# Kernel optimization log

Measured on AMD Instinct MI355X. Metric: run time of the kernel, lower is better.

The kernel has to match this reference:

```python
import jax, jax.numpy as jnp
import numpy as np

DIM = 1024
E = 8
K = 2
EPS = 1e-5

def _ln(x, g, b):
    mu = jnp.mean(x, axis=-1, keepdims=True)
    var = jnp.mean(jnp.square(x - mu), axis=-1, keepdims=True)
    return (x - mu) * jax.lax.rsqrt(var + EPS) * g + b

def setup_inputs() -> dict:
    key = jax.random.key(0)
    ks = jax.random.split(key, 8)
    H = 2 * DIM
    s_in = 1.0 / np.sqrt(DIM)
    s_h = 1.0 / np.sqrt(H)
    return {
        "x": jax.random.normal(ks[0], (2, 2048, DIM), dtype=jnp.float32),
        "gate_w": jax.random.uniform(ks[1], (DIM, E), minval=-s_in, maxval=s_in, dtype=jnp.float32),
        "w1": jax.random.uniform(ks[2], (E, DIM, H), minval=-s_in, maxval=s_in, dtype=jnp.float32),
        "b1": jax.random.uniform(ks[3], (E, H), minval=-s_in, maxval=s_in, dtype=jnp.float32),
        "ln1_g": jnp.ones((E, H), dtype=jnp.float32),
        "ln1_b": jnp.zeros((E, H), dtype=jnp.float32),
        "w2": jax.random.uniform(ks[4], (E, H, DIM), minval=-s_h, maxval=s_h, dtype=jnp.float32),
        "b2": jax.random.uniform(ks[5], (E, DIM), minval=-s_h, maxval=s_h, dtype=jnp.float32),
        "ln_g": jnp.ones((DIM,), dtype=jnp.float32),
        "ln_b": jnp.zeros((DIM,), dtype=jnp.float32),
    }

def reference(x, gate_w, w1, b1, ln1_g, ln1_b, w2, b2, ln_g, ln_b):
    shape = x.shape
    xf = x.reshape(-1, shape[-1])                      # [T, D]
    gates = jax.nn.softmax(xf @ gate_w, axis=-1)       # [T, E]
    topw, topi = jax.lax.top_k(gates, K)               # [T, K]
    topw = topw / jnp.sum(topw, axis=-1, keepdims=True)
    # combine weights per expert: [T, E]
    combine = jnp.sum(topw[:, :, None] * jax.nn.one_hot(topi, E, dtype=xf.dtype), axis=1)
    # run all experts on all tokens (vectorized grouped GEMM), combine by gate mask
    h = jnp.einsum('td,edh->teh', xf, w1) + b1          # [T, E, 2D]
    h = _ln(h, ln1_g, ln1_b)
    h = jax.nn.gelu(h, approximate=False)
    y = jnp.einsum('teh,ehd->ted', h, w2) + b2          # [T, E, D]
    out = jnp.einsum('ted,te->td', y, combine)          # [T, D]
    out = _ln(out + xf, ln_g, ln_b)
    return out.reshape(shape)
```

## Files before the change

kernel.cpp:

```cpp
#include <hip/hip_runtime.h>
#include <hip/hip_bf16.h>

#define DIMX 1024
#define HID  2048
#define NE   8
#define NT   4096
#define NPAIR 8192

typedef __attribute__((ext_vector_type(8))) __bf16 bf16x8;
typedef __attribute__((ext_vector_type(4))) float f32x4;

__device__ inline unsigned short f2bf(float f) {
  union { float f; unsigned u; } v; v.f = f;
  unsigned r = v.u + 0x7FFFu + ((v.u >> 16) & 1u);
  return (unsigned short)(r >> 16);
}
__device__ inline float bf2f(unsigned short h) {
  union { unsigned u; float f; } v; v.u = ((unsigned)h) << 16;
  return v.f;
}

__device__ __forceinline__ void gload_lds16(const unsigned short* g, unsigned short* l) {
  __builtin_amdgcn_global_load_lds(
      (const __attribute__((address_space(1))) unsigned int*)g,
      (__attribute__((address_space(3))) unsigned int*)l, 16, 0, 0);
}

#define O_CNT   0u
#define O_OFFS  256u
#define O_TOK   1024u
#define O_TK    (O_TOK + 131072u)
#define O_PW    (O_TK + 131072u)
#define O_TI    (O_PW + 131072u)
#define O_TW    (O_TI + 32768u)
#define O_XBF   524288u
#define O_W1T   16777216u
#define O_W2T   50331648u
#define O_H     83886080u
#define O_Y     117440512u

__global__ __launch_bounds__(64) void k_gate_top2(const float* __restrict__ x,
                                                  const float* __restrict__ gw,
                                                  int* __restrict__ ti,
                                                  float* __restrict__ tw) {
  int t = blockIdx.x;
  int lane = threadIdx.x;
  float p[NE];
#pragma unroll
  for (int e = 0; e < NE; e++) p[e] = 0.f;
  const float* xr = x + (size_t)t * DIMX;
  for (int j = 0; j < DIMX / 64; j++) {
    int d = lane + j * 64;
    float xv = xr[d];
    const float4* g4 = (const float4*)(gw + (size_t)d * NE);
    float4 a = g4[0], b = g4[1];
    p[0] += xv * a.x; p[1] += xv * a.y; p[2] += xv * a.z; p[3] += xv * a.w;
    p[4] += xv * b.x; p[5] += xv * b.y; p[6] += xv * b.z; p[7] += xv * b.w;
  }
#pragma unroll
  for (int e = 0; e < NE; e++)
#pragma unroll
    for (int off = 32; off > 0; off >>= 1) p[e] += __shfl_xor(p[e], off);
  if (lane == 0) {
    int ia = 0; float va = p[0];
#pragma unroll
    for (int e = 1; e < NE; e++) if (p[e] > va) { va = p[e]; ia = e; }
    int ib = -1; float vb = -3.0e38f;
#pragma unroll
    for (int e = 0; e < NE; e++) { if (e == ia) continue; if (p[e] > vb) { vb = p[e]; ib = e; } }
    float w0 = 1.f / (1.f + expf(vb - va));
    ti[t * 2] = ia;     tw[t * 2] = w0;
    ti[t * 2 + 1] = ib; tw[t * 2 + 1] = 1.f - w0;
  }
}

__global__ __launch_bounds__(512) void k_build(const int* __restrict__ ti,
                                               const float* __restrict__ tw,
                                               int* __restrict__ cnt, int* __restrict__ offs,
                                               int* __restrict__ ptok, int* __restrict__ ptk,
                                               float* __restrict__ pw) {
  __shared__ int scnt[NE];
  __shared__ int soffs[NE + 1];
  int wid = threadIdx.x >> 6;
  int lane = threadIdx.x & 63;
  int c = 0;
  for (int p = lane; p < NPAIR; p += 64) c += (ti[p] == wid) ? 1 : 0;
#pragma unroll
  for (int off = 32; off > 0; off >>= 1) c += __shfl_xor(c, off);
  if (lane == 0) scnt[wid] = c;
  __syncthreads();
  if (threadIdx.x == 0) {
    int s = 0;
    for (int e = 0; e < NE; e++) { soffs[e] = s; s += scnt[e]; }
    soffs[NE] = s;
  }
  __syncthreads();
  if (threadIdx.x < NE) {
    cnt[threadIdx.x] = scnt[threadIdx.x];
    offs[threadIdx.x] = soffs[threadIdx.x];
  }
  if (threadIdx.x == 0) offs[NE] = soffs[NE];
  int base = 0;
  for (int p0 = 0; p0 < NPAIR; p0 += 64) {
    int p = p0 + lane;
    bool m = (ti[p] == wid);
    unsigned long long mask = __ballot(m);
    if (m) {
      int pos = base + __popcll(mask & ((1ull << lane) - 1ull));
      ptok[wid * NT + pos] = p >> 1;
      ptk[wid * NT + pos] = p;
      pw[wid * NT + pos] = tw[p];
    }
    base += __popcll(mask);
  }
}

__global__ __launch_bounds__(256) void k_transpose_cvt(const float* __restrict__ in,
                                                       unsigned short* __restrict__ out,
                                                       int R, int C) {
  __shared__ float tile[32][33];
  int e = blockIdx.z;
  const float* ip = in + (size_t)e * R * C;
  unsigned short* op = out + (size_t)e * R * C;
  int tx = threadIdx.x & 31, ty = threadIdx.x >> 5;
  int c = blockIdx.x * 32 + tx;
  int r0 = blockIdx.y * 32;
#pragma unroll
  for (int i = 0; i < 4; i++) tile[ty + i * 8][tx] = ip[(size_t)(r0 + ty + i * 8) * C + c];
  __syncthreads();
  int r = r0 + tx;
#pragma unroll
  for (int i = 0; i < 4; i++)
    op[(size_t)(blockIdx.x * 32 + ty + i * 8) * R + r] = f2bf(tile[tx][ty + i * 8]);
}

__global__ __launch_bounds__(256) void k_cvt(const float* __restrict__ in,
                                             unsigned short* __restrict__ out, int n4) {
  int i = blockIdx.x * blockDim.x + threadIdx.x;
  if (i < n4) {
    float4 v = ((const float4*)in)[i];
    ushort4 o; o.x = f2bf(v.x); o.y = f2bf(v.y); o.z = f2bf(v.z); o.w = f2bf(v.w);
    ((ushort4*)out)[i] = o;
  }
}

#define BM 128
#define BN 128
#define BK 32

__global__ __launch_bounds__(256) void k_gemm1(
    const unsigned short* __restrict__ xbf,
    const unsigned short* __restrict__ w1t,
    const float* __restrict__ bias1,
    const int* __restrict__ cnt, const int* __restrict__ offs,
    const int* __restrict__ ptok,
    unsigned short* __restrict__ hpre)
{
  int e = blockIdx.z;
  int n_e = cnt[e];
  int row0 = blockIdx.y * BM;
  if (row0 >= n_e) return;
  int col0 = blockIdx.x * BN;
  int offs_e = offs[e];

  __shared__ __align__(16) unsigned short As[BM][BK];
  __shared__ __align__(16) unsigned short Bs[BN][BK];

  int tid = threadIdx.x;
  int lane = tid & 63, wid = tid >> 6;
  int wr = wid >> 1, wc = wid & 1;
  int quad = lane >> 4, m16 = lane & 15;

  int i4 = lane >> 2, kc = lane & 3;
  int ga0 = row0 + wid * 32 + i4;      if (ga0 >= n_e) ga0 = n_e - 1;
  int ga1 = row0 + wid * 32 + 16 + i4; if (ga1 >= n_e) ga1 = n_e - 1;
  int t0 = ptok[e * NT + ga0];
  int t1 = ptok[e * NT + ga1];
  const unsigned short* a0p = xbf + (size_t)t0 * DIMX + kc * 8;
  const unsigned short* a1p = xbf + (size_t)t1 * DIMX + kc * 8;
  const unsigned short* bb = w1t + (size_t)e * HID * DIMX;
  const unsigned short* b0p = bb + (size_t)(col0 + wid * 32 + i4) * DIMX + kc * 8;
  const unsigned short* b1p = bb + (size_t)(col0 + wid * 32 + 16 + i4) * DIMX + kc * 8;
  unsigned short* lA0 = &As[wid * 32][0];
  unsigned short* lA1 = &As[wid * 32 + 16][0];
  unsigned short* lB0 = &Bs[wid * 32][0];
  unsigned short* lB1 = &Bs[wid * 32 + 16][0];

  f32x4 acc[4][4];
#pragma unroll
  for (int i = 0; i < 4; i++)
#pragma unroll
    for (int j = 0; j < 4; j++) acc[i][j] = (f32x4)(0.f);

  for (int k0 = 0; k0 < DIMX; k0 += BK) {
    __syncthreads();
    gload_lds16(a0p + k0, lA0);
    gload_lds16(a1p + k0, lA1);
    gload_lds16(b0p + k0, lB0);
    gload_lds16(b1p + k0, lB1);
    __syncthreads();
    bf16x8 af[4], bfr[4];
#pragma unroll
    for (int i = 0; i < 4; i++) af[i]  = *(const bf16x8*)&As[wr * 64 + i * 16 + m16][quad * 8];
#pragma unroll
    for (int i = 0; i < 4; i++) bfr[i] = *(const bf16x8*)&Bs[wc * 64 + i * 16 + m16][quad * 8];
#pragma unroll
    for (int i = 0; i < 4; i++)
#pragma unroll
      for (int j = 0; j < 4; j++)
        acc[i][j] = __builtin_amdgcn_mfma_f32_16x16x32_bf16(af[i], bfr[j], acc[i][j], 0, 0, 0);
  }

#pragma unroll
  for (int i = 0; i < 4; i++) {
#pragma unroll
    for (int r = 0; r < 4; r++) {
      int rl = wr * 64 + i * 16 + quad * 4 + r;
      int g = row0 + rl;
      if (g < n_e) {
        size_t rowbase = (size_t)(offs_e + g) * HID;
#pragma unroll
        for (int j = 0; j < 4; j++) {
          int colg = col0 + wc * 64 + j * 16 + m16;
          float val = acc[i][j][r] + bias1[e * HID + colg];
          hpre[rowbase + colg] = f2bf(val);
        }
      }
    }
  }
}

__global__ __launch_bounds__(256) void k_ln_gelu(unsigned short* __restrict__ h,
                                                 const float* __restrict__ g1,
                                                 const float* __restrict__ bb1,
                                                 const int* __restrict__ offs) {
  __shared__ float sbuf[4];
  int row = blockIdx.x;
  int tid = threadIdx.x;
  int e = 0;
#pragma unroll
  for (int i = 1; i < NE; i++) if (row >= offs[i]) e = i;
  unsigned short* p = h + (size_t)row * HID;
  float v[8];
#pragma unroll
  for (int i = 0; i < 8; i++) v[i] = bf2f(p[tid + i * 256]);
  float s = 0.f;
#pragma unroll
  for (int i = 0; i < 8; i++) s += v[i];
#pragma unroll
  for (int off = 32; off > 0; off >>= 1) s += __shfl_xor(s, off);
  if ((tid & 63) == 0) sbuf[tid >> 6] = s;
  __syncthreads();
  float mean = (sbuf[0] + sbuf[1] + sbuf[2] + sbuf[3]) * (1.f / HID);
  float sq = 0.f;
#pragma unroll
  for (int i = 0; i < 8; i++) { float d = v[i] - mean; sq += d * d; }
#pragma unroll
  for (int off = 32; off > 0; off >>= 1) sq += __shfl_xor(sq, off);
  __syncthreads();
  if ((tid & 63) == 0) sbuf[tid >> 6] = sq;
  __syncthreads();
  float var = (sbuf[0] + sbuf[1] + sbuf[2] + sbuf[3]) * (1.f / HID);
  float rstd = rsqrtf(var + 1e-5f);
#pragma unroll
  for (int i = 0; i < 8; i++) {
    int d = tid + i * 256;
    float xn = (v[i] - mean) * rstd * g1[(size_t)e * HID + d] + bb1[(size_t)e * HID + d];
    float ge = 0.5f * xn * (1.f + erff(xn * 0.7071067811865476f));
    p[d] = f2bf(ge);
  }
}

__global__ __launch_bounds__(256) void k_gemm2(
    const unsigned short* __restrict__ hb,
    const unsigned short* __restrict__ w2t,
    const float* __restrict__ bias2,
    const int* __restrict__ cnt, const int* __restrict__ offs,
    const int* __restrict__ ptk, const float* __restrict__ pw,
    float* __restrict__ ybuf)
{
  int e = blockIdx.z;
  int n_e = cnt[e];
  int row0 = blockIdx.y * BM;
  if (row0 >= n_e) return;
  int col0 = blockIdx.x * BN;
  int offs_e = offs[e];

  __shared__ __align__(16) unsigned short As[BM][BK];
  __shared__ __align__(16) unsigned short Bs[BN][BK];

  int tid = threadIdx.x;
  int lane = tid & 63, wid = tid >> 6;
  int wr = wid >> 1, wc = wid & 1;
  int quad = lane >> 4, m16 = lane & 15;

  int i4 = lane >> 2, kc = lane & 3;
  int ga0 = row0 + wid * 32 + i4;      if (ga0 >= n_e) ga0 = n_e - 1;
  int ga1 = row0 + wid * 32 + 16 + i4; if (ga1 >= n_e) ga1 = n_e - 1;
  const unsigned short* a0p = hb + (size_t)(offs_e + ga0) * HID + kc * 8;
  const unsigned short* a1p = hb + (size_t)(offs_e + ga1) * HID + kc * 8;
  const unsigned short* bb = w2t + (size_t)e * DIMX * HID;
  const unsigned short* b0p = bb + (size_t)(col0 + wid * 32 + i4) * HID + kc * 8;
  const unsigned short* b1p = bb + (size_t)(col0 + wid * 32 + 16 + i4) * HID + kc * 8;
  unsigned short* lA0 = &As[wid * 32][0];
  unsigned short* lA1 = &As[wid * 32 + 16][0];
  unsigned short* lB0 = &Bs[wid * 32][0];
  unsigned short* lB1 = &Bs[wid * 32 + 16][0];

  f32x4 acc[4][4];
#pragma unroll
  for (int i = 0; i < 4; i++)
#pragma unroll
    for (int j = 0; j < 4; j++) acc[i][j] = (f32x4)(0.f);

  for (int k0 = 0; k0 < HID; k0 += BK) {
    __syncthreads();
    gload_lds16(a0p + k0, lA0);
    gload_lds16(a1p + k0, lA1);
    gload_lds16(b0p + k0, lB0);
    gload_lds16(b1p + k0, lB1);
    __syncthreads();
    bf16x8 af[4], bfr[4];
#pragma unroll
    for (int i = 0; i < 4; i++) af[i]  = *(const bf16x8*)&As[wr * 64 + i * 16 + m16][quad * 8];
#pragma unroll
    for (int i = 0; i < 4; i++) bfr[i] = *(const bf16x8*)&Bs[wc * 64 + i * 16 + m16][quad * 8];
#pragma unroll
    for (int i = 0; i < 4; i++)
#pragma unroll
      for (int j = 0; j < 4; j++)
        acc[i][j] = __builtin_amdgcn_mfma_f32_16x16x32_bf16(af[i], bfr[j], acc[i][j], 0, 0, 0);
  }

#pragma unroll
  for (int i = 0; i < 4; i++) {
#pragma unroll
    for (int r = 0; r < 4; r++) {
      int rl = wr * 64 + i * 16 + quad * 4 + r;
      int g = row0 + rl;
      if (g < n_e) {
        int pi = e * NT + g;
        float w = pw[pi];
        size_t obase = (size_t)ptk[pi] * DIMX;
#pragma unroll
        for (int j = 0; j < 4; j++) {
          int colg = col0 + wc * 64 + j * 16 + m16;
          ybuf[obase + colg] = (acc[i][j][r] + bias2[e * DIMX + colg]) * w;
        }
      }
    }
  }
}

__global__ __launch_bounds__(256) void k_final(const float* __restrict__ yb,
                                               const float* __restrict__ x,
                                               const float* __restrict__ lg,
                                               const float* __restrict__ lb,
                                               float* __restrict__ out) {
  __shared__ float sbuf[4];
  int t = blockIdx.x, tid = threadIdx.x;
  const float4* y0 = (const float4*)(yb + (size_t)t * 2 * DIMX);
  const float4* y1 = y0 + DIMX / 4;
  const float4* x4 = (const float4*)(x + (size_t)t * DIMX);
  float4 a = y0[tid], b = y1[tid], c = x4[tid];
  float4 v; v.x = a.x + b.x + c.x; v.y = a.y + b.y + c.y;
  v.z = a.z + b.z + c.z; v.w = a.w + b.w + c.w;
  float s = v.x + v.y + v.z + v.w;
#pragma unroll
  for (int off = 32; off > 0; off >>= 1) s += __shfl_xor(s, off);
  if ((tid & 63) == 0) sbuf[tid >> 6] = s;
  __syncthreads();
  float mean = (sbuf[0] + sbuf[1] + sbuf[2] + sbuf[3]) * (1.f / DIMX);
  float dx = v.x - mean, dy = v.y - mean, dz = v.z - mean, dw = v.w - mean;
  float sq = dx * dx + dy * dy + dz * dz + dw * dw;
#pragma unroll
  for (int off = 32; off > 0; off >>= 1) sq += __shfl_xor(sq, off);
  __syncthreads();
  if ((tid & 63) == 0) sbuf[tid >> 6] = sq;
  __syncthreads();
  float var = (sbuf[0] + sbuf[1] + sbuf[2] + sbuf[3]) * (1.f / DIMX);
  float rstd = rsqrtf(var + 1e-5f);
  float4 g = ((const float4*)lg)[tid], bb = ((const float4*)lb)[tid];
  float4 o; o.x = dx * rstd * g.x + bb.x; o.y = dy * rstd * g.y + bb.y;
  o.z = dz * rstd * g.z + bb.z; o.w = dw * rstd * g.w + bb.w;
  ((float4*)(out + (size_t)t * DIMX))[tid] = o;
}

extern "C" void kernel_launch(void* const* d_in, const int* in_sizes, int n_in,
                              void* d_out, int out_size, void* d_ws, size_t ws_size,
                              hipStream_t stream) {
  const float* x     = (const float*)d_in[0];
  const float* gw    = (const float*)d_in[1];
  const float* w1    = (const float*)d_in[2];
  const float* b1    = (const float*)d_in[3];
  const float* ln1g  = (const float*)d_in[4];
  const float* ln1b  = (const float*)d_in[5];
  const float* w2    = (const float*)d_in[6];
  const float* b2    = (const float*)d_in[7];
  const float* lng   = (const float*)d_in[8];
  const float* lnb   = (const float*)d_in[9];
  float* out = (float*)d_out;

  char* ws = (char*)d_ws;
  int* cnt  = (int*)(ws + O_CNT);
  int* offs = (int*)(ws + O_OFFS);
  int* ptok = (int*)(ws + O_TOK);
  int* ptk  = (int*)(ws + O_TK);
  float* pw = (float*)(ws + O_PW);
  int* ti   = (int*)(ws + O_TI);
  float* tw = (float*)(ws + O_TW);
  unsigned short* xbf = (unsigned short*)(ws + O_XBF);
  unsigned short* w1t = (unsigned short*)(ws + O_W1T);
  unsigned short* w2t = (unsigned short*)(ws + O_W2T);
  unsigned short* hpre = (unsigned short*)(ws + O_H);
  float* ybuf = (float*)(ws + O_Y);

  hipLaunchKernelGGL(k_gate_top2, dim3(NT), dim3(64), 0, stream, x, gw, ti, tw);
  hipLaunchKernelGGL(k_build, dim3(1), dim3(512), 0, stream, ti, tw, cnt, offs, ptok, ptk, pw);
  hipLaunchKernelGGL(k_cvt, dim3(NT * DIMX / 4 / 256), dim3(256), 0, stream, x, xbf, NT * DIMX / 4);
  hipLaunchKernelGGL(k_transpose_cvt, dim3(HID / 32, DIMX / 32, NE), dim3(256), 0, stream,
                     w1, w1t, DIMX, HID);
  hipLaunchKernelGGL(k_transpose_cvt, dim3(DIMX / 32, HID / 32, NE), dim3(256), 0, stream,
                     w2, w2t, HID, DIMX);
  hipLaunchKernelGGL(k_gemm1, dim3(HID / BN, NT / BM, NE), dim3(256), 0, stream,
                     xbf, w1t, b1, cnt, offs, ptok, hpre);
  hipLaunchKernelGGL(k_ln_gelu, dim3(NPAIR), dim3(256), 0, stream, hpre, ln1g, ln1b, offs);
  hipLaunchKernelGGL(k_gemm2, dim3(DIMX / BN, NT / BM, NE), dim3(256), 0, stream,
                     hpre, w2t, b2, cnt, offs, ptk, pw, ybuf);
  hipLaunchKernelGGL(k_final, dim3(NT), dim3(256), 0, stream, ybuf, x, lng, lnb, out);
}
```

Before: 415.8 us.

## Compact grouped-GEMM grid into per-expert strip list and fuse x conversion into gating

Replaces the dense (col, NT/BM, NE) GEMM grids, where most blocks exit early, with a compact list of 128-row strips built in k_build, padding each expert's rows to a multiple of 128. The bf16 conversion of x is fused into the gating kernel. The weight transpose uses 64x64 tiles with vectorized loads and stores, and LN+GELU is vectorized and looks up its expert from the strip table. This removes many empty blocks and one launch, in exchange for a serial strip-building step and padded row space that the LN kernel has to skip.

```diff
diff --git a/kernel.cpp b/kernel.cpp
--- a/kernel.cpp
+++ b/kernel.cpp
@@ -6,6 +6,7 @@
 #define NE   8
 #define NT   4096
 #define NPAIR 8192
+#define MAXSTRIP 72
 
 typedef __attribute__((ext_vector_type(8))) __bf16 bf16x8;
 typedef __attribute__((ext_vector_type(4))) float f32x4;
@@ -27,35 +28,49 @@
 }
 
 #define O_CNT   0u
-#define O_OFFS  256u
 #define O_TOK   1024u
-#define O_TK    (O_TOK + 131072u)
-#define O_PW    (O_TK + 131072u)
-#define O_TI    (O_PW + 131072u)
-#define O_TW    (O_TI + 32768u)
+#define O_TK    132096u
+#define O_PW    263168u
+#define O_TI    394240u
+#define O_TW    427008u
+#define O_POFF  459776u
+#define O_SE    459904u
+#define O_SR0   460416u
 #define O_XBF   524288u
 #define O_W1T   16777216u
 #define O_W2T   50331648u
 #define O_H     83886080u
-#define O_Y     117440512u
-
-__global__ __launch_bounds__(64) void k_gate_top2(const float* __restrict__ x,
+#define O_Y     121634816u
+
+__global__ __launch_bounds__(256) void k_gate_cvt(const float* __restrict__ x,
                                                   const float* __restrict__ gw,
+                                                  unsigned short* __restrict__ xbf,
                                                   int* __restrict__ ti,
                                                   float* __restrict__ tw) {
-  int t = blockIdx.x;
-  int lane = threadIdx.x;
+  int t = blockIdx.x * 4 + (threadIdx.x >> 6);
+  int lane = threadIdx.x & 63;
+  const float4* xr = (const float4*)(x + (size_t)t * DIMX);
+  ushort4* xo = (ushort4*)(xbf + (size_t)t * DIMX);
   float p[NE];
 #pragma unroll
   for (int e = 0; e < NE; e++) p[e] = 0.f;
-  const float* xr = x + (size_t)t * DIMX;
-  for (int j = 0; j < DIMX / 64; j++) {
-    int d = lane + j * 64;
-    float xv = xr[d];
-    const float4* g4 = (const float4*)(gw + (size_t)d * NE);
-    float4 a = g4[0], b = g4[1];
-    p[0] += xv * a.x; p[1] += xv * a.y; p[2] += xv * a.z; p[3] += xv * a.w;
-    p[4] += xv * b.x; p[5] += xv * b.y; p[6] += xv * b.z; p[7] += xv * b.w;
+#pragma unroll
+  for (int j = 0; j < 4; j++) {
+    int idx4 = j * 64 + lane;
+    float4 v = xr[idx4];
+    ushort4 o; o.x = f2bf(v.x); o.y = f2bf(v.y); o.z = f2bf(v.z); o.w = f2bf(v.w);
+    xo[idx4] = o;
+    const float4* gp = (const float4*)(gw + (size_t)(idx4 * 4) * NE);
+    float4 gA = gp[0], gB = gp[1], gC = gp[2], gD = gp[3];
+    float4 gE = gp[4], gF = gp[5], gG = gp[6], gH = gp[7];
+    p[0] += v.x * gA.x + v.y * gC.x + v.z * gE.x + v.w * gG.x;
+    p[1] += v.x * gA.y + v.y * gC.y + v.z * gE.y + v.w * gG.y;
+    p[2] += v.x * gA.z + v.y * gC.z + v.z * gE.z + v.w * gG.z;
+    p[3] += v.x * gA.w + v.y * gC.w + v.z * gE.w + v.w * gG.w;
+    p[4] += v.x * gB.x + v.y * gD.x + v.z * gF.x + v.w * gH.x;
+    p[5] += v.x * gB.y + v.y * gD.y + v.z * gF.y + v.w * gH.y;
+    p[6] += v.x * gB.z + v.y * gD.z + v.z * gF.z + v.w * gH.z;
+    p[7] += v.x * gB.w + v.y * gD.w + v.z * gF.w + v.w * gH.w;
   }
 #pragma unroll
   for (int e = 0; e < NE; e++)
@@ -76,34 +91,39 @@
 
 __global__ __launch_bounds__(512) void k_build(const int* __restrict__ ti,
                                                const float* __restrict__ tw,
-                                               int* __restrict__ cnt, int* __restrict__ offs,
+                                               int* __restrict__ cnt,
+                                               int* __restrict__ poffs,
+                                               int* __restrict__ s_e, int* __restrict__ s_r0,
                                                int* __restrict__ ptok, int* __restrict__ ptk,
                                                float* __restrict__ pw) {
+  __shared__ int sti[NPAIR];
   __shared__ int scnt[NE];
-  __shared__ int soffs[NE + 1];
+  for (int i = threadIdx.x; i < NPAIR; i += 512) sti[i] = ti[i];
+  __syncthreads();
   int wid = threadIdx.x >> 6;
   int lane = threadIdx.x & 63;
   int c = 0;
-  for (int p = lane; p < NPAIR; p += 64) c += (ti[p] == wid) ? 1 : 0;
+  for (int p = lane; p < NPAIR; p += 64) c += (sti[p] == wid) ? 1 : 0;
 #pragma unroll
   for (int off = 32; off > 0; off >>= 1) c += __shfl_xor(c, off);
   if (lane == 0) scnt[wid] = c;
   __syncthreads();
   if (threadIdx.x == 0) {
-    int s = 0;
-    for (int e = 0; e < NE; e++) { soffs[e] = s; s += scnt[e]; }
-    soffs[NE] = s;
-  }
-  __syncthreads();
-  if (threadIdx.x < NE) {
-    cnt[threadIdx.x] = scnt[threadIdx.x];
-    offs[threadIdx.x] = soffs[threadIdx.x];
-  }
-  if (threadIdx.x == 0) offs[NE] = soffs[NE];
+    int s = 0, pacc = 0;
+    for (int e = 0; e < NE; e++) {
+      cnt[e] = scnt[e];
+      poffs[e] = pacc;
+      int ns = (scnt[e] + 127) >> 7;
+      for (int k = 0; k < ns; k++) { s_e[s] = e; s_r0[s] = k * 128; s++; }
+      pacc += ns * 128;
+    }
+    poffs[NE] = pacc;
+    for (; s < MAXSTRIP; s++) { s_e[s] = -1; s_r0[s] = 0; }
+  }
   int base = 0;
   for (int p0 = 0; p0 < NPAIR; p0 += 64) {
     int p = p0 + lane;
-    bool m = (ti[p] == wid);
+    bool m = (sti[p] == wid);
     unsigned long long mask = __ballot(m);
     if (m) {
       int pos = base + __popcll(mask & ((1ull << lane) - 1ull));
@@ -118,29 +138,29 @@
 __global__ __launch_bounds__(256) void k_transpose_cvt(const float* __restrict__ in,
                                                        unsigned short* __restrict__ out,
                                                        int R, int C) {
-  __shared__ float tile[32][33];
+  __shared__ float tile[64][73];
   int e = blockIdx.z;
   const float* ip = in + (size_t)e * R * C;
   unsigned short* op = out + (size_t)e * R * C;
-  int tx = threadIdx.x & 31, ty = threadIdx.x >> 5;
-  int c = blockIdx.x * 32 + tx;
-  int r0 = blockIdx.y * 32;
-#pragma unroll
-  for (int i = 0; i < 4; i++) tile[ty + i * 8][tx] = ip[(size_t)(r0 + ty + i * 8) * C + c];
-  __syncthreads();
-  int r = r0 + tx;
-#pragma unroll
-  for (int i = 0; i < 4; i++)
-    op[(size_t)(blockIdx.x * 32 + ty + i * 8) * R + r] = f2bf(tile[tx][ty + i * 8]);
-}
-
-__global__ __launch_bounds__(256) void k_cvt(const float* __restrict__ in,
-                                             unsigned short* __restrict__ out, int n4) {
-  int i = blockIdx.x * blockDim.x + threadIdx.x;
-  if (i < n4) {
-    float4 v = ((const float4*)in)[i];
-    ushort4 o; o.x = f2bf(v.x); o.y = f2bf(v.y); o.z = f2bf(v.z); o.w = f2bf(v.w);
-    ((ushort4*)out)[i] = o;
+  int c0 = blockIdx.x * 64, r0 = blockIdx.y * 64;
+  int tx = threadIdx.x & 15, ty = threadIdx.x >> 4;
+#pragma unroll
+  for (int i = 0; i < 4; i++) {
+    int row = ty + i * 16;
+    float4 v = *(const float4*)(ip + (size_t)(r0 + row) * C + c0 + tx * 4);
+    tile[row][tx * 4] = v.x; tile[row][tx * 4 + 1] = v.y;
+    tile[row][tx * 4 + 2] = v.z; tile[row][tx * 4 + 3] = v.w;
+  }
+  __syncthreads();
+  int rx = threadIdx.x & 15, cy = threadIdx.x >> 4;
+  int r_off = rx * 4;
+#pragma unroll
+  for (int i = 0; i < 4; i++) {
+    int cc = cy + i * 16;
+    ushort4 h;
+    h.x = f2bf(tile[r_off][cc]);     h.y = f2bf(tile[r_off + 1][cc]);
+    h.z = f2bf(tile[r_off + 2][cc]); h.w = f2bf(tile[r_off + 3][cc]);
+    *(ushort4*)(op + (size_t)(c0 + cc) * R + r0 + r_off) = h;
   }
 }
 
@@ -152,16 +172,18 @@
     const unsigned short* __restrict__ xbf,
     const unsigned short* __restrict__ w1t,
     const float* __restrict__ bias1,
-    const int* __restrict__ cnt, const int* __restrict__ offs,
+    const int* __restrict__ cnt, const int* __restrict__ s_e,
+    const int* __restrict__ s_r0, const int* __restrict__ poffs,
     const int* __restrict__ ptok,
     unsigned short* __restrict__ hpre)
 {
-  int e = blockIdx.z;
+  int s = blockIdx.y;
+  int e = s_e[s];
+  if (e < 0) return;
+  int r0e = s_r0[s];
   int n_e = cnt[e];
-  int row0 = blockIdx.y * BM;
-  if (row0 >= n_e) return;
+  int pbase = poffs[e];
   int col0 = blockIdx.x * BN;
-  int offs_e = offs[e];
 
   __shared__ __align__(16) unsigned short As[BM][BK];
   __shared__ __align__(16) unsigned short Bs[BN][BK];
@@ -172,8 +194,8 @@
   int quad = lane >> 4, m16 = lane & 15;
 
   int i4 = lane >> 2, kc = lane & 3;
-  int ga0 = row0 + wid * 32 + i4;      if (ga0 >= n_e) ga0 = n_e - 1;
-  int ga1 = row0 + wid * 32 + 16 + i4; if (ga1 >= n_e) ga1 = n_e - 1;
+  int ga0 = r0e + wid * 32 + i4;      if (ga0 >= n_e) ga0 = n_e - 1;
+  int ga1 = r0e + wid * 32 + 16 + i4; if (ga1 >= n_e) ga1 = n_e - 1;
   int t0 = ptok[e * NT + ga0];
   int t1 = ptok[e * NT + ga1];
   const unsigned short* a0p = xbf + (size_t)t0 * DIMX + kc * 8;
@@ -215,10 +237,9 @@
   for (int i = 0; i < 4; i++) {
 #pragma unroll
     for (int r = 0; r < 4; r++) {
-      int rl = wr * 64 + i * 16 + quad * 4 + r;
-      int g = row0 + rl;
+      int g = r0e + wr * 64 + i * 16 + quad * 4 + r;
       if (g < n_e) {
-        size_t rowbase = (size_t)(offs_e + g) * HID;
+        size_t rowbase = (size_t)(pbase + g) * HID;
 #pragma unroll
         for (int j = 0; j < 4; j++) {
           int colg = col0 + wc * 64 + j * 16 + m16;
@@ -233,17 +254,18 @@
 __global__ __launch_bounds__(256) void k_ln_gelu(unsigned short* __restrict__ h,
                                                  const float* __restrict__ g1,
                                                  const float* __restrict__ bb1,
-                                                 const int* __restrict__ offs) {
+                                                 const int* __restrict__ s_e) {
   __shared__ float sbuf[4];
   int row = blockIdx.x;
+  int e = s_e[row >> 7];
+  if (e < 0) return;
   int tid = threadIdx.x;
-  int e = 0;
-#pragma unroll
-  for (int i = 1; i < NE; i++) if (row >= offs[i]) e = i;
   unsigned short* p = h + (size_t)row * HID;
+  ushort4 u0 = ((const ushort4*)p)[tid * 2];
+  ushort4 u1 = ((const ushort4*)p)[tid * 2 + 1];
   float v[8];
-#pragma unroll
-  for (int i = 0; i < 8; i++) v[i] = bf2f(p[tid + i * 256]);
+  v[0] = bf2f(u0.x); v[1] = bf2f(u0.y); v[2] = bf2f(u0.z); v[3] = bf2f(u0.w);
+  v[4] = bf2f(u1.x); v[5] = bf2f(u1.y); v[6] = bf2f(u1.z); v[7] = bf2f(u1.w);
   float s = 0.f;
 #pragma unroll
   for (int i = 0; i < 8; i++) s += v[i];
@@ -262,29 +284,41 @@
   __syncthreads();
   float var = (sbuf[0] + sbuf[1] + sbuf[2] + sbuf[3]) * (1.f / HID);
   float rstd = rsqrtf(var + 1e-5f);
+  const float4* gg = (const float4*)(g1 + (size_t)e * HID);
+  const float4* gb = (const float4*)(bb1 + (size_t)e * HID);
+  float4 ga = gg[tid * 2], gbv = gg[tid * 2 + 1];
+  float4 ba = gb[tid * 2], bbv = gb[tid * 2 + 1];
+  float gn[8] = {ga.x, ga.y, ga.z, ga.w, gbv.x, gbv.y, gbv.z, gbv.w};
+  float bn[8] = {ba.x, ba.y, ba.z, ba.w, bbv.x, bbv.y, bbv.z, bbv.w};
+  unsigned short o[8];
 #pragma unroll
   for (int i = 0; i < 8; i++) {
-    int d = tid + i * 256;
-    float xn = (v[i] - mean) * rstd * g1[(size_t)e * HID + d] + bb1[(size_t)e * HID + d];
+    float xn = (v[i] - mean) * rstd * gn[i] + bn[i];
     float ge = 0.5f * xn * (1.f + erff(xn * 0.7071067811865476f));
-    p[d] = f2bf(ge);
-  }
+    o[i] = f2bf(ge);
+  }
+  ushort4 s0 = {o[0], o[1], o[2], o[3]};
+  ushort4 s1 = {o[4], o[5], o[6], o[7]};
+  ((ushort4*)p)[tid * 2] = s0;
+  ((ushort4*)p)[tid * 2 + 1] = s1;
 }
 
 __global__ __launch_bounds__(256) void k_gemm2(
     const unsigned short* __restrict__ hb,
     const unsigned short* __restrict__ w2t,
     const float* __restrict__ bias2,
-    const int* __restrict__ cnt, const int* __restrict__ offs,
+    const int* __restrict__ cnt, const int* __restrict__ s_e,
+    const int* __restrict__ s_r0, const int* __restrict__ poffs,
     const int* __restrict__ ptk, const float* __restrict__ pw,
     float* __restrict__ ybuf)
 {
-  int e = blockIdx.z;
+  int s = blockIdx.y;
+  int e = s_e[s];
+  if (e < 0) return;
+  int r0e = s_r0[s];
   int n_e = cnt[e];
-  int row0 = blockIdx.y * BM;
-  if (row0 >= n_e) return;
+  int pbase = poffs[e];
   int col0 = blockIdx.x * BN;
-  int offs_e = offs[e];
 
   __shared__ __align__(16) unsigned short As[BM][BK];
   __shared__ __align__(16) unsigned short Bs[BN][BK];
@@ -295,10 +329,10 @@
   int quad = lane >> 4, m16 = lane & 15;
 
   int i4 = lane >> 2, kc = lane & 3;
-  int ga0 = row0 + wid * 32 + i4;      if (ga0 >= n_e) ga0 = n_e - 1;
-  int ga1 = row0 + wid * 32 + 16 + i4; if (ga1 >= n_e) ga1 = n_e - 1;
-  const unsigned short* a0p = hb + (size_t)(offs_e + ga0) * HID + kc * 8;
-  const unsigned short* a1p = hb + (size_t)(offs_e + ga1) * HID + kc * 8;
+  int ga0 = r0e + wid * 32 + i4;      if (ga0 >= n_e) ga0 = n_e - 1;
+  int ga1 = r0e + wid * 32 + 16 + i4; if (ga1 >= n_e) ga1 = n_e - 1;
+  const unsigned short* a0p = hb + (size_t)(pbase + ga0) * HID + kc * 8;
+  const unsigned short* a1p = hb + (size_t)(pbase + ga1) * HID + kc * 8;
   const unsigned short* bb = w2t + (size_t)e * DIMX * HID;
   const unsigned short* b0p = bb + (size_t)(col0 + wid * 32 + i4) * HID + kc * 8;
   const unsigned short* b1p = bb + (size_t)(col0 + wid * 32 + 16 + i4) * HID + kc * 8;
@@ -336,8 +370,7 @@
   for (int i = 0; i < 4; i++) {
 #pragma unroll
     for (int r = 0; r < 4; r++) {
-      int rl = wr * 64 + i * 16 + quad * 4 + r;
-      int g = row0 + rl;
+      int g = r0e + wr * 64 + i * 16 + quad * 4 + r;
       if (g < n_e) {
         int pi = e * NT + g;
         float w = pw[pi];
@@ -402,30 +435,32 @@
   float* out = (float*)d_out;
 
   char* ws = (char*)d_ws;
-  int* cnt  = (int*)(ws + O_CNT);
-  int* offs = (int*)(ws + O_OFFS);
-  int* ptok = (int*)(ws + O_TOK);
-  int* ptk  = (int*)(ws + O_TK);
-  float* pw = (float*)(ws + O_PW);
-  int* ti   = (int*)(ws + O_TI);
-  float* tw = (float*)(ws + O_TW);
-  unsigned short* xbf = (unsigned short*)(ws + O_XBF);
-  unsigned short* w1t = (unsigned short*)(ws + O_W1T);
-  unsigned short* w2t = (unsigned short*)(ws + O_W2T);
+  int* cnt   = (int*)(ws + O_CNT);
+  int* ptok  = (int*)(ws + O_TOK);
+  int* ptk   = (int*)(ws + O_TK);
+  float* pw  = (float*)(ws + O_PW);
+  int* ti    = (int*)(ws + O_TI);
+  float* tw  = (float*)(ws + O_TW);
+  int* poffs = (int*)(ws + O_POFF);
+  int* s_e   = (int*)(ws + O_SE);
+  int* s_r0  = (int*)(ws + O_SR0);
+  unsigned short* xbf  = (unsigned short*)(ws + O_XBF);
+  unsigned short* w1t  = (unsigned short*)(ws + O_W1T);
+  unsigned short* w2t  = (unsigned short*)(ws + O_W2T);
   unsigned short* hpre = (unsigned short*)(ws + O_H);
   float* ybuf = (float*)(ws + O_Y);
 
-  hipLaunchKernelGGL(k_gate_top2, dim3(NT), dim3(64), 0, stream, x, gw, ti, tw);
-  hipLaunchKernelGGL(k_build, dim3(1), dim3(512), 0, stream, ti, tw, cnt, offs, ptok, ptk, pw);
-  hipLaunchKernelGGL(k_cvt, dim3(NT * DIMX / 4 / 256), dim3(256), 0, stream, x, xbf, NT * DIMX / 4);
-  hipLaunchKernelGGL(k_transpose_cvt, dim3(HID / 32, DIMX / 32, NE), dim3(256), 0, stream,
+  hipLaunchKernelGGL(k_gate_cvt, dim3(NT / 4), dim3(256), 0, stream, x, gw, xbf, ti, tw);
+  hipLaunchKernelGGL(k_build, dim3(1), dim3(512), 0, stream, ti, tw, cnt, poffs, s_e, s_r0,
+                     ptok, ptk, pw);
+  hipLaunchKernelGGL(k_transpose_cvt, dim3(HID / 64, DIMX / 64, NE), dim3(256), 0, stream,
                      w1, w1t, DIMX, HID);
-  hipLaunchKernelGGL(k_transpose_cvt, dim3(DIMX / 32, HID / 32, NE), dim3(256), 0, stream,
+  hipLaunchKernelGGL(k_transpose_cvt, dim3(DIMX / 64, HID / 64, NE), dim3(256), 0, stream,
                      w2, w2t, HID, DIMX);
-  hipLaunchKernelGGL(k_gemm1, dim3(HID / BN, NT / BM, NE), dim3(256), 0, stream,
-                     xbf, w1t, b1, cnt, offs, ptok, hpre);
-  hipLaunchKernelGGL(k_ln_gelu, dim3(NPAIR), dim3(256), 0, stream, hpre, ln1g, ln1b, offs);
-  hipLaunchKernelGGL(k_gemm2, dim3(DIMX / BN, NT / BM, NE), dim3(256), 0, stream,
-                     hpre, w2t, b2, cnt, offs, ptk, pw, ybuf);
+  hipLaunchKernelGGL(k_gemm1, dim3(HID / BN, MAXSTRIP), dim3(256), 0, stream,
+                     xbf, w1t, b1, cnt, s_e, s_r0, poffs, ptok, hpre);
+  hipLaunchKernelGGL(k_ln_gelu, dim3(MAXSTRIP * BM), dim3(256), 0, stream, hpre, ln1g, ln1b, s_e);
+  hipLaunchKernelGGL(k_gemm2, dim3(DIMX / BN, MAXSTRIP), dim3(256), 0, stream,
+                     hpre, w2t, b2, cnt, s_e, s_r0, poffs, ptk, pw, ybuf);
   hipLaunchKernelGGL(k_final, dim3(NT), dim3(256), 0, stream, ybuf, x, lng, lnb, out);
 }
```

Measured after the change: 401.9 us. -3.3%, faster.
